# Performance work log

Hardware: AMD Instinct MI355X
Metric: run time of the kernel (lower is better)

The kernel has to match this reference:

```python
import jax, jax.numpy as jnp
import numpy as np

HEADS = 8
C_HEAD = 64  # head dim == in_dim of x
P0, P1 = 2, 3  # adaptive pool output


def setup_inputs() -> dict:
    key = jax.random.key(0)
    ks = jax.random.split(key, 8)
    b, c, h, w = 16, 64, 64, 96
    m, d = 6, 192
    inner = HEADS * C_HEAD  # 512
    return {
        "x": jax.random.normal(ks[0], (b, c, h, w), dtype=jnp.float32),
        "z": jax.random.normal(ks[1], (b, m, d), dtype=jnp.float32),
        "conv_w": jax.random.normal(ks[2], (192, c), dtype=jnp.float32) * 0.02,
        "conv_b": jax.random.normal(ks[3], (192,), dtype=jnp.float32) * 0.02,
        "wq": jax.random.normal(ks[4], (d, inner), dtype=jnp.float32) * 0.02,
        "bq": jax.random.normal(ks[5], (inner,), dtype=jnp.float32) * 0.02,
        "wo": jax.random.normal(ks[6], (inner, d), dtype=jnp.float32) * 0.02,
        "bo": jax.random.normal(ks[7], (d,), dtype=jnp.float32) * 0.02,
    }


def reference(x, z, conv_w, conv_b, wq, bq, wo, bo):
    b, c, h, w = x.shape
    _, m, d = z.shape
    # 1x1 conv (pointwise GEMM over channels) + bias
    xp = jnp.einsum('bchw,oc->bohw', x, conv_w) + conv_b[None, :, None, None]
    # AdaptiveAvgPool2d((2,3)) with exact divisibility -> block mean
    xp = xp.reshape(b, 192, P0, h // P0, P1, w // P1).mean(axis=(3, 5))  # [b,192,2,3]
    # view(b, d, m) then permute(0,2,1) -> [b, m, d]
    z = z + xp.reshape(b, d, m).transpose(0, 2, 1)
    # k = v: view(b, h*w, c), repeat heads along last dim, view(b, heads, h*w, c)
    # (row-major reshape reproduces torch .view semantics exactly)
    kv = jnp.tile(x.reshape(b, h * w, c), (1, 1, HEADS)).reshape(b, HEADS, h * w, C_HEAD)
    # q = Linear(dim, heads*c) then view(b, heads, m, c)
    q = (z @ wq + bq).reshape(b, HEADS, m, C_HEAD)
    scale = C_HEAD ** -0.5
    dots = jnp.einsum('bhmc,bhlc->bhml', q, kv) * scale  # [b,h,m,l]
    attn = jax.nn.softmax(dots, axis=-1)
    out = jnp.einsum('bhml,bhlc->bhmc', attn, kv)
    out = out.transpose(0, 2, 1, 3).reshape(b, m, HEADS * C_HEAD)  # b m (h c)
    return z + out @ wo + bo
```

## Files before the change

kernel.cpp:

```cpp
#include <hip/hip_runtime.h>

#define NB 16
#define NC 64
#define NM 6
#define ND 192
#define NHEADS 8
#define NCH 64
#define NINNER 512
#define PLANE 6144
#define XB (NC*PLANE)
#define NKEY 768
#define NCHUNK 8
#define CK 96
#define KP 68
#define SP 100

__global__ __launch_bounds__(256) void pool_kernel(const float* __restrict__ x,
                                                   float* __restrict__ xmean) {
    int bc = blockIdx.x;
    const float4* p = (const float4*)(x + (size_t)bc * PLANE);
    int tid = threadIdx.x;
    float acc[6] = {0.f,0.f,0.f,0.f,0.f,0.f};
    #pragma unroll
    for (int k = 0; k < 6; ++k) {
        int idx4 = tid + k * 256;
        int hh = idx4 / 24;
        int w4 = idx4 - hh * 24;
        int j = (hh >> 5) * 3 + (w4 >> 3);
        float4 v = p[idx4];
        acc[j] += v.x + v.y + v.z + v.w;
    }
    int lane = tid & 63, wave = tid >> 6;
    #pragma unroll
    for (int j = 0; j < 6; ++j) {
        float v = acc[j];
        for (int off = 32; off > 0; off >>= 1) v += __shfl_down(v, off, 64);
        acc[j] = v;
    }
    __shared__ float part[4][6];
    if (lane == 0) {
        #pragma unroll
        for (int j = 0; j < 6; ++j) part[wave][j] = acc[j];
    }
    __syncthreads();
    if (tid < 6) {
        float s = part[0][tid] + part[1][tid] + part[2][tid] + part[3][tid];
        xmean[bc * 6 + tid] = s * (1.0f / 1024.0f);
    }
}

__global__ __launch_bounds__(256) void zq_kernel(const float* __restrict__ z,
                                                 const float* __restrict__ conv_w,
                                                 const float* __restrict__ conv_b,
                                                 const float* __restrict__ wq,
                                                 const float* __restrict__ bq,
                                                 const float* __restrict__ xmean,
                                                 float* __restrict__ znew,
                                                 float* __restrict__ qr) {
    int blk = blockIdx.x;
    int cgrp = blk & 7, bm = blk >> 3;
    int b = bm / NM, m = bm - b * NM;
    int tid = threadIdx.x;
    __shared__ float xm[NC];
    __shared__ float zn[ND];
    __shared__ float qpart[3][64];
    if (tid < NC) xm[tid] = xmean[(b * NC + tid) * NM + m];
    __syncthreads();
    if (tid < ND) {
        float a = conv_b[tid];
        const float4* wr4 = (const float4*)(conv_w + tid * NC);
        #pragma unroll
        for (int c4 = 0; c4 < 16; ++c4) {
            float4 w = wr4[c4];
            a += w.x * xm[c4 * 4 + 0] + w.y * xm[c4 * 4 + 1]
               + w.z * xm[c4 * 4 + 2] + w.w * xm[c4 * 4 + 3];
        }
        float v = z[bm * ND + tid] + a;
        zn[tid] = v;
        if (cgrp == 0) znew[bm * ND + tid] = v;
    }
    __syncthreads();
    int colL = tid & 63, ks = tid >> 6;
    int col = cgrp * 64 + colL;
    float a = (ks == 0) ? bq[col] : 0.f;
    int d0 = ks * 48;
    #pragma unroll
    for (int d = d0; d < d0 + 48; ++d) a += zn[d] * wq[d * NINNER + col];
    if (ks > 0) qpart[ks - 1][colL] = a;
    __syncthreads();
    if (ks == 0) {
        float tot = a + qpart[0][colL] + qpart[1][colL] + qpart[2][colL];
        int t = m * 8 + cgrp;
        qr[b * (48 * 64) + t * 64 + colL] = tot;
    }
}

__global__ __launch_bounds__(256, 4) void fattn_kernel(const float* __restrict__ x,
                                                       const float* __restrict__ qr,
                                                       float* __restrict__ po,
                                                       float* __restrict__ ps) {
    int blk = blockIdx.x;
    int chunk = blk & 7, bh = blk >> 3;
    int head = bh & 7, b = bh >> 3;
    int tid = threadIdx.x;
    __shared__ float k_lds[CK][KP];
    __shared__ float q_lds[NM][KP];
    __shared__ float s_lds[NM][SP];
    __shared__ float4 pvp4[4][NM][16];
    const float* kbase = x + (size_t)b * XB + (size_t)(head * NKEY + chunk * CK) * NCH;

    for (int i = tid; i < NM * NCH; i += 256) {
        int mi = i >> 6, ch = i & 63;
        q_lds[mi][ch] = qr[b * (48 * 64) + (head * NM + mi) * 64 + ch];
    }
    const float4* k4 = (const float4*)kbase;
    #pragma unroll
    for (int r = 0; r < 6; ++r) {
        int i = tid + r * 256;
        int row = i >> 4, c4 = i & 15;
        float4 v = k4[i];
        *(float4*)&k_lds[row][c4 * 4] = v;
    }
    __syncthreads();

    if (tid < 96) {
        int u = tid;
        float a[NM] = {0.f,0.f,0.f,0.f,0.f,0.f};
        #pragma unroll
        for (int c4 = 0; c4 < 16; ++c4) {
            float4 kv = *(const float4*)&k_lds[u][c4 * 4];
            #pragma unroll
            for (int mo = 0; mo < NM; ++mo) {
                float4 qv = *(const float4*)&q_lds[mo][c4 * 4];
                a[mo] += kv.x*qv.x + kv.y*qv.y + kv.z*qv.z + kv.w*qv.w;
            }
        }
        #pragma unroll
        for (int mo = 0; mo < NM; ++mo) s_lds[mo][u] = __expf(a[mo] * 0.125f);
    }
    __syncthreads();

    int lane = tid & 63, wave = tid >> 6;

    #pragma unroll
    for (int rb = 0; rb < 2; ++rb) {
        int mi = rb * 4 + wave;
        if (mi < NM) {
            float v = s_lds[mi][lane] + ((lane < 32) ? s_lds[mi][64 + lane] : 0.f);
            for (int msk = 1; msk < 64; msk <<= 1) v += __shfl_xor(v, msk, 64);
            if (lane == 0) ps[blk * NM + mi] = v;
        }
    }

    {
        int qd = tid & 15, rg = tid >> 4;
        float4 acc4[NM];
        #pragma unroll
        for (int mo = 0; mo < NM; ++mo) acc4[mo] = make_float4(0.f,0.f,0.f,0.f);
        int u0 = rg * 6;
        #pragma unroll
        for (int j = 0; j < 6; ++j) {
            int u = u0 + j;
            float4 kv = *(const float4*)&k_lds[u][qd * 4];
            #pragma unroll
            for (int mo = 0; mo < NM; ++mo) {
                float s = s_lds[mo][u];
                acc4[mo].x += s * kv.x; acc4[mo].y += s * kv.y;
                acc4[mo].z += s * kv.z; acc4[mo].w += s * kv.w;
            }
        }
        #pragma unroll
        for (int mo = 0; mo < NM; ++mo) {
            acc4[mo].x += __shfl_xor(acc4[mo].x, 16, 64);
            acc4[mo].y += __shfl_xor(acc4[mo].y, 16, 64);
            acc4[mo].z += __shfl_xor(acc4[mo].z, 16, 64);
            acc4[mo].w += __shfl_xor(acc4[mo].w, 16, 64);
            acc4[mo].x += __shfl_xor(acc4[mo].x, 32, 64);
            acc4[mo].y += __shfl_xor(acc4[mo].y, 32, 64);
            acc4[mo].z += __shfl_xor(acc4[mo].z, 32, 64);
            acc4[mo].w += __shfl_xor(acc4[mo].w, 32, 64);
        }
        if (lane < 16) {
            #pragma unroll
            for (int mo = 0; mo < NM; ++mo) pvp4[wave][mo][qd] = acc4[mo];
        }
    }
    __syncthreads();

    if (tid < 96) {
        int mo = tid >> 4, qd = tid & 15;
        float4 o = pvp4[0][mo][qd];
        float4 o1 = pvp4[1][mo][qd];
        float4 o2 = pvp4[2][mo][qd];
        float4 o3 = pvp4[3][mo][qd];
        o.x += o1.x + o2.x + o3.x;
        o.y += o1.y + o2.y + o3.y;
        o.z += o1.z + o2.z + o3.z;
        o.w += o1.w + o2.w + o3.w;
        *(float4*)&po[(size_t)blk * (NM * NCH) + mo * NCH + qd * 4] = o;
    }
}

__global__ __launch_bounds__(256) void proj_kernel(const float* __restrict__ znew,
                                                   const float* __restrict__ po,
                                                   const float* __restrict__ ps,
                                                   const float* __restrict__ wo,
                                                   const float* __restrict__ bo,
                                                   float* __restrict__ out) {
    int blk = blockIdx.x;
    int cgrp = blk & 3, bm = blk >> 2;
    int b = bm / NM, m = bm - b * NM;
    int tid = threadIdx.x;
    __shared__ float4 orow4[128];
    __shared__ float4 part4[16][12];

    if (tid < 128) {
        int h = tid >> 4, c16 = tid & 15;
        int base = (b * NHEADS + h) * NCHUNK;
        const float4* po4 = (const float4*)po;
        float4 n = make_float4(0.f, 0.f, 0.f, 0.f);
        float den = 0.f;
        #pragma unroll
        for (int c = 0; c < NCHUNK; ++c) {
            float4 v = po4[(size_t)(base + c) * 96 + m * 16 + c16];
            n.x += v.x; n.y += v.y; n.z += v.z; n.w += v.w;
            den += ps[(base + c) * NM + m];
        }
        float inv = 1.0f / den;
        n.x *= inv; n.y *= inv; n.z *= inv; n.w *= inv;
        orow4[tid] = n;
    }
    __syncthreads();

    if (tid < 192) {
        int g4 = tid % 12, ks = tid / 12;
        int cb = cgrp * 12 + g4;
        const float4* wo4 = (const float4*)wo;
        const float* orow = (const float*)orow4;
        float4 acc = make_float4(0.f, 0.f, 0.f, 0.f);
        int i0 = ks * 32;
        #pragma unroll 8
        for (int i = i0; i < i0 + 32; ++i) {
            float s = orow[i];
            float4 w = wo4[i * 48 + cb];
            acc.x += s * w.x; acc.y += s * w.y; acc.z += s * w.z; acc.w += s * w.w;
        }
        part4[ks][g4] = acc;
    }
    __syncthreads();

    if (tid < 48) {
        int g4 = tid >> 2, j = tid & 3;
        float s = 0.f;
        #pragma unroll
        for (int ks = 0; ks < 16; ++ks) s += ((const float*)&part4[ks][g4])[j];
        int col = cgrp * 48 + tid;
        out[bm * ND + col] = s + bo[col] + znew[bm * ND + col];
    }
}

extern "C" void kernel_launch(void* const* d_in, const int* in_sizes, int n_in,
                              void* d_out, int out_size, void* d_ws, size_t ws_size,
                              hipStream_t stream) {
    const float* x      = (const float*)d_in[0];
    const float* z      = (const float*)d_in[1];
    const float* conv_w = (const float*)d_in[2];
    const float* conv_b = (const float*)d_in[3];
    const float* wq     = (const float*)d_in[4];
    const float* bq     = (const float*)d_in[5];
    const float* wo     = (const float*)d_in[6];
    const float* bo     = (const float*)d_in[7];
    float* out = (float*)d_out;

    float* ws    = (float*)d_ws;
    float* xmean = ws;
    float* znew  = ws + 6144;
    float* qr    = ws + 24576;
    float* po    = ws + 73728;
    float* ps    = ws + 466944;

    pool_kernel<<<NB*NC, 256, 0, stream>>>(x, xmean);
    zq_kernel<<<NB*NM*8, 256, 0, stream>>>(z, conv_w, conv_b, wq, bq, xmean, znew, qr);
    fattn_kernel<<<NB*NHEADS*NCHUNK, 256, 0, stream>>>(x, qr, po, ps);
    proj_kernel<<<NB*NM*4, 256, 0, stream>>>(znew, po, ps, wo, bo, out);
}
```

Measured before the change: 32.12 us.

## Restructure attention PV stage per-channel and swizzle QK LDS reads

The PV accumulation is reorganized so that two waves each compute three query rows for one channel per lane across all 96 keys. This removes the cross-lane shuffle reductions, the pvp4 staging buffer and one block barrier. The other two waves compute the softmax row sums in parallel. LDS padding is dropped in favor of a rotating column index in the QK loop to avoid bank conflicts, which lowers LDS use and allows the launch-bounds occupancy hint to rise from 4 to 5. The trade-off is that half the waves do the PV work serially over 96 keys, which risks a longer critical path.

```diff
diff --git a/kernel.cpp b/kernel.cpp
--- a/kernel.cpp
+++ b/kernel.cpp
@@ -12,8 +12,6 @@
 #define NKEY 768
 #define NCHUNK 8
 #define CK 96
-#define KP 68
-#define SP 100
 
 __global__ __launch_bounds__(256) void pool_kernel(const float* __restrict__ x,
                                                    float* __restrict__ xmean) {
@@ -95,7 +93,7 @@
     }
 }
 
-__global__ __launch_bounds__(256, 4) void fattn_kernel(const float* __restrict__ x,
+__global__ __launch_bounds__(256, 5) void fattn_kernel(const float* __restrict__ x,
                                                        const float* __restrict__ qr,
                                                        float* __restrict__ po,
                                                        float* __restrict__ ps) {
@@ -103,10 +101,9 @@
     int chunk = blk & 7, bh = blk >> 3;
     int head = bh & 7, b = bh >> 3;
     int tid = threadIdx.x;
-    __shared__ float k_lds[CK][KP];
-    __shared__ float q_lds[NM][KP];
-    __shared__ float s_lds[NM][SP];
-    __shared__ float4 pvp4[4][NM][16];
+    __shared__ float k_lds[CK][NCH];
+    __shared__ float q_lds[NM][NCH];
+    __shared__ float s_lds[NM][CK];
     const float* kbase = x + (size_t)b * XB + (size_t)(head * NKEY + chunk * CK) * NCH;
 
     for (int i = tid; i < NM * NCH; i += 256) {
@@ -128,10 +125,11 @@
         float a[NM] = {0.f,0.f,0.f,0.f,0.f,0.f};
         #pragma unroll
         for (int c4 = 0; c4 < 16; ++c4) {
-            float4 kv = *(const float4*)&k_lds[u][c4 * 4];
+            int cc = ((c4 + u) & 15) * 4;
+            float4 kv = *(const float4*)&k_lds[u][cc];
             #pragma unroll
             for (int mo = 0; mo < NM; ++mo) {
-                float4 qv = *(const float4*)&q_lds[mo][c4 * 4];
+                float4 qv = *(const float4*)&q_lds[mo][cc];
                 a[mo] += kv.x*qv.x + kv.y*qv.y + kv.z*qv.z + kv.w*qv.w;
             }
         }
@@ -142,62 +140,34 @@
 
     int lane = tid & 63, wave = tid >> 6;
 
-    #pragma unroll
-    for (int rb = 0; rb < 2; ++rb) {
-        int mi = rb * 4 + wave;
-        if (mi < NM) {
+    if (wave < 2) {
+        int ch = lane, m0 = wave * 3;
+        float a0 = 0.f, a1 = 0.f, a2 = 0.f;
+        #pragma unroll
+        for (int u0 = 0; u0 < CK; u0 += 4) {
+            float4 s0 = *(const float4*)&s_lds[m0 + 0][u0];
+            float4 s1 = *(const float4*)&s_lds[m0 + 1][u0];
+            float4 s2 = *(const float4*)&s_lds[m0 + 2][u0];
+            float kv0 = k_lds[u0 + 0][ch];
+            float kv1 = k_lds[u0 + 1][ch];
+            float kv2 = k_lds[u0 + 2][ch];
+            float kv3 = k_lds[u0 + 3][ch];
+            a0 += s0.x*kv0 + s0.y*kv1 + s0.z*kv2 + s0.w*kv3;
+            a1 += s1.x*kv0 + s1.y*kv1 + s1.z*kv2 + s1.w*kv3;
+            a2 += s2.x*kv0 + s2.y*kv1 + s2.z*kv2 + s2.w*kv3;
+        }
+        float* pob = po + (size_t)blk * (NM * NCH);
+        pob[(m0 + 0) * NCH + ch] = a0;
+        pob[(m0 + 1) * NCH + ch] = a1;
+        pob[(m0 + 2) * NCH + ch] = a2;
+    } else {
+        #pragma unroll
+        for (int rnd = 0; rnd < 3; ++rnd) {
+            int mi = rnd * 2 + (wave - 2);
             float v = s_lds[mi][lane] + ((lane < 32) ? s_lds[mi][64 + lane] : 0.f);
             for (int msk = 1; msk < 64; msk <<= 1) v += __shfl_xor(v, msk, 64);
             if (lane == 0) ps[blk * NM + mi] = v;
         }
-    }
-
-    {
-        int qd = tid & 15, rg = tid >> 4;
-        float4 acc4[NM];
-        #pragma unroll
-        for (int mo = 0; mo < NM; ++mo) acc4[mo] = make_float4(0.f,0.f,0.f,0.f);
-        int u0 = rg * 6;
-        #pragma unroll
-        for (int j = 0; j < 6; ++j) {
-            int u = u0 + j;
-            float4 kv = *(const float4*)&k_lds[u][qd * 4];
-            #pragma unroll
-            for (int mo = 0; mo < NM; ++mo) {
-                float s = s_lds[mo][u];
-                acc4[mo].x += s * kv.x; acc4[mo].y += s * kv.y;
-                acc4[mo].z += s * kv.z; acc4[mo].w += s * kv.w;
-            }
-        }
-        #pragma unroll
-        for (int mo = 0; mo < NM; ++mo) {
-            acc4[mo].x += __shfl_xor(acc4[mo].x, 16, 64);
-            acc4[mo].y += __shfl_xor(acc4[mo].y, 16, 64);
-            acc4[mo].z += __shfl_xor(acc4[mo].z, 16, 64);
-            acc4[mo].w += __shfl_xor(acc4[mo].w, 16, 64);
-            acc4[mo].x += __shfl_xor(acc4[mo].x, 32, 64);
-            acc4[mo].y += __shfl_xor(acc4[mo].y, 32, 64);
-            acc4[mo].z += __shfl_xor(acc4[mo].z, 32, 64);
-            acc4[mo].w += __shfl_xor(acc4[mo].w, 32, 64);
-        }
-        if (lane < 16) {
-            #pragma unroll
-            for (int mo = 0; mo < NM; ++mo) pvp4[wave][mo][qd] = acc4[mo];
-        }
-    }
-    __syncthreads();
-
-    if (tid < 96) {
-        int mo = tid >> 4, qd = tid & 15;
-        float4 o = pvp4[0][mo][qd];
-        float4 o1 = pvp4[1][mo][qd];
-        float4 o2 = pvp4[2][mo][qd];
-        float4 o3 = pvp4[3][mo][qd];
-        o.x += o1.x + o2.x + o3.x;
-        o.y += o1.y + o2.y + o3.y;
-        o.z += o1.z + o2.z + o3.z;
-        o.w += o1.w + o2.w + o3.w;
-        *(float4*)&po[(size_t)blk * (NM * NCH) + mo * NCH + qd * 4] = o;
     }
 }
 
```

Result: faster. 31.36 us (median of 2 runs) (-2.4%).
